# Kernel optimization log

Measured on AMD Instinct MI355X. Metric: run time of the kernel, lower is better.

The kernel has to match this reference:

```python
import jax, jax.numpy as jnp
import numpy as np

L, B, S, H, NH, HD = 2, 2, 1024, 768, 12, 64
E, K, F, V = 8, 2, 3072, 50257
THETA = 10000.0
EPS = 1e-5


def setup_inputs() -> dict:
    key = jax.random.key(0)
    ks = iter(jax.random.split(key, 40))
    def nrm(shape):
        return jax.random.normal(next(ks), shape, jnp.float32) * 0.02
    return {
        "input_ids": jax.random.randint(next(ks), (B, S), 0, V),
        "emb": nrm((V, H)),
        "ln1_w": jnp.ones((L, H)), "ln1_b": jnp.zeros((L, H)),
        "ln2_w": jnp.ones((L, H)), "ln2_b": jnp.zeros((L, H)),
        "lnf_w": jnp.ones((H,)), "lnf_b": jnp.zeros((H,)),
        "Wq": nrm((L, H, H)), "bq": jnp.zeros((L, H)),
        "Wk": nrm((L, H, H)), "bk": jnp.zeros((L, H)),
        "Wv": nrm((L, H, H)), "bv": jnp.zeros((L, H)),
        "Wo": nrm((L, H, H)), "bo": jnp.zeros((L, H)),
        "Wr": nrm((L, H, E)), "br": jnp.zeros((L, E)),
        "W1": nrm((L, E, H, F)), "b1": jnp.zeros((L, E, F)),
        "W2": nrm((L, E, F, H)), "b2": jnp.zeros((L, E, H)),
    }


def _layer_norm(x, w, b):
    m = x.mean(-1, keepdims=True)
    v = ((x - m) ** 2).mean(-1, keepdims=True)
    return (x - m) * jax.lax.rsqrt(v + EPS) * w + b


def _rotate_half(x):
    x1, x2 = jnp.split(x, 2, axis=-1)
    return jnp.concatenate([-x2, x1], axis=-1)


def _forward(input_ids, emb, ln1_w, ln1_b, ln2_w, ln2_b, lnf_w, lnf_b,
             Wq, bq, Wk, bk, Wv, bv, Wo, bo, Wr, br, W1, b1, W2, b2):
    x = emb[input_ids]  # [B,S,H]

    # RoPE tables [1,1,S,HD]
    inv_freq = 1.0 / (THETA ** (jnp.arange(0, HD, 2, dtype=jnp.float32) / HD))
    freqs = jnp.arange(S, dtype=jnp.float32)[:, None] * inv_freq[None, :]
    ang = jnp.concatenate([freqs, freqs], axis=-1)
    cos = jnp.cos(ang)[None, None].astype(x.dtype)
    sin = jnp.sin(ang)[None, None].astype(x.dtype)

    causal = jnp.where(jnp.tril(jnp.ones((S, S), dtype=bool)), 0.0, -1e9)
    causal = causal[None, None].astype(x.dtype)

    scale = 1.0 / np.sqrt(HD)
    for l in range(L):
        # --- attention block ---
        h = _layer_norm(x, ln1_w[l], ln1_b[l])
        q = (h @ Wq[l] + bq[l]).reshape(B, S, NH, HD).transpose(0, 2, 1, 3)
        k = (h @ Wk[l] + bk[l]).reshape(B, S, NH, HD).transpose(0, 2, 1, 3)
        v = (h @ Wv[l] + bv[l]).reshape(B, S, NH, HD).transpose(0, 2, 1, 3)
        q = q * cos + _rotate_half(q) * sin
        k = k * cos + _rotate_half(k) * sin
        scores = jnp.einsum('bhqd,bhkd->bhqk', q, k) * scale + causal
        attn = jax.nn.softmax(scores, axis=-1)
        o = jnp.einsum('bhqk,bhkd->bhqd', attn, v)
        o = o.transpose(0, 2, 1, 3).reshape(B, S, H)
        x = x + (o @ Wo[l] + bo[l])

        # --- MoE feed-forward block ---
        h = _layer_norm(x, ln2_w[l], ln2_b[l]).reshape(-1, H)  # [N,H]
        router_probs = jax.nn.softmax(h @ Wr[l] + br[l], axis=-1)  # [N,E]
        tp, ti = jax.lax.top_k(router_probs, K)
        tp = tp / (tp.sum(-1, keepdims=True) + 1e-9)
        # combine weights per expert (equiv. to the per-slot scatter loop)
        w = (jax.nn.one_hot(ti, E, dtype=h.dtype) * tp[..., None]).sum(1)  # [N,E]
        a = jax.nn.gelu(jnp.einsum('nh,ehf->nef', h, W1[l]) + b1[l], approximate=False)
        oe = jnp.einsum('nef,efh->neh', a, W2[l]) + b2[l]
        ff = jnp.einsum('ne,neh->nh', w, oe)
        x = x + ff.reshape(B, S, H)

    x = _layer_norm(x, lnf_w, lnf_b)
    logits = jnp.einsum('bsh,vh->bsv', x, emb)  # tied lm_head
    return logits


def reference(input_ids, emb, ln1_w, ln1_b, ln2_w, ln2_b, lnf_w, lnf_b,
              Wq, bq, Wk, bk, Wv, bv, Wo, bo, Wr, br, W1, b1, W2, b2):
    return _forward(input_ids, emb, ln1_w, ln1_b, ln2_w, ln2_b, lnf_w, lnf_b,
                    Wq, bq, Wk, bk, Wv, bv, Wo, bo, Wr, br, W1, b1, W2, b2)
```

## Files before the change

### kernel.cpp

```cpp
#include <hip/hip_runtime.h>
#include <stdint.h>

constexpr int L = 2, Bb = 2, S = 1024, H = 768, NHd = 12, HD = 64;
constexpr int E = 8, F = 3072, V = 50257;
constexpr int NTOK = Bb * S;
constexpr int NSLOT = NTOK * 2;
constexpr float EPSLN = 1e-5f;

typedef __attribute__((ext_vector_type(4))) float f32x4;
typedef __attribute__((ext_vector_type(8))) short s16x8;

#define DEVI __device__ __forceinline__

DEVI float bf2f(short u) {
  union { float f; uint32_t i; } c; c.i = ((uint32_t)(uint16_t)u) << 16; return c.f;
}
DEVI short f2bf(float f) {
  union { float f; uint32_t i; } c; c.f = f;
  uint32_t x = c.i;
  uint32_t r = (x + 0x7fffu + ((x >> 16) & 1u)) >> 16;
  return (short)r;
}

DEVI void gload16(const void* g, void* l) {
  __builtin_amdgcn_global_load_lds(g, l, 16, 0, 0);
}

DEVI float gelu1(float g) { return 0.5f * g * (1.f + erff(g * 0.70710678118f)); }

__global__ void k_f32_to_bf16(const float* __restrict__ in, short* __restrict__ out, long n4) {
  long i = (long)blockIdx.x * blockDim.x + threadIdx.x;
  if (i >= n4) return;
  long base = i * 4;
  f32x4 v = *(const f32x4*)(in + base);
  short4 o;
  o.x = f2bf(v.x); o.y = f2bf(v.y); o.z = f2bf(v.z); o.w = f2bf(v.w);
  *(short4*)(out + base) = o;
}

__global__ void k_transpose_bf16(const float* __restrict__ in, short* __restrict__ out,
                                 int R, int C, long inBS, long outBS) {
  __shared__ float tile[32][33];
  const float* src = in + (size_t)blockIdx.z * inBS;
  short* dst = out + (size_t)blockIdx.z * outBS;
  int r0 = blockIdx.y * 32, c0 = blockIdx.x * 32;
  int tx = threadIdx.x, ty = threadIdx.y;
#pragma unroll
  for (int i = 0; i < 32; i += 8) {
    int r = r0 + ty + i, c = c0 + tx;
    if (r < R && c < C) tile[ty + i][tx] = src[(size_t)r * C + c];
  }
  __syncthreads();
#pragma unroll
  for (int i = 0; i < 32; i += 8) {
    int c = c0 + ty + i, r = r0 + tx;
    if (r < R && c < C) dst[(size_t)c * R + r] = f2bf(tile[tx][ty + i]);
  }
}

__global__ void k_transpose_split(const float* __restrict__ in, short* __restrict__ oh,
                                  short* __restrict__ ol, int R, int C, long inBS,
                                  long outBS) {
  __shared__ float tile[32][33];
  const float* src = in + (size_t)blockIdx.z * inBS;
  short* dh = oh + (size_t)blockIdx.z * outBS;
  short* dl = ol + (size_t)blockIdx.z * outBS;
  int r0 = blockIdx.y * 32, c0 = blockIdx.x * 32;
  int tx = threadIdx.x, ty = threadIdx.y;
#pragma unroll
  for (int i = 0; i < 32; i += 8) {
    int r = r0 + ty + i, c = c0 + tx;
    if (r < R && c < C) tile[ty + i][tx] = src[(size_t)r * C + c];
  }
  __syncthreads();
#pragma unroll
  for (int i = 0; i < 32; i += 8) {
    int c = c0 + ty + i, r = r0 + tx;
    if (r < R && c < C) {
      float v = tile[tx][ty + i];
      short hi = f2bf(v);
      short lo = f2bf(v - bf2f(hi));
      dh[(size_t)c * R + r] = hi;
      dl[(size_t)c * R + r] = lo;
    }
  }
}

__global__ void k_transpose_split3(const float* __restrict__ in, short* __restrict__ o0,
                                   short* __restrict__ o1, short* __restrict__ o2,
                                   int R, int C) {
  __shared__ float tile[32][33];
  int r0 = blockIdx.y * 32, c0 = blockIdx.x * 32;
  int tx = threadIdx.x, ty = threadIdx.y;
#pragma unroll
  for (int i = 0; i < 32; i += 8) {
    int r = r0 + ty + i, c = c0 + tx;
    if (r < R && c < C) tile[ty + i][tx] = in[(size_t)r * C + c];
  }
  __syncthreads();
#pragma unroll
  for (int i = 0; i < 32; i += 8) {
    int c = c0 + ty + i, r = r0 + tx;
    if (r < R && c < C) {
      float v = tile[tx][ty + i];
      short t0 = f2bf(v);
      float rr = v - bf2f(t0);
      short t1 = f2bf(rr);
      short t2 = f2bf(rr - bf2f(t1));
      o0[(size_t)c * R + r] = t0;
      o1[(size_t)c * R + r] = t1;
      o2[(size_t)c * R + r] = t2;
    }
  }
}

__global__ void k_wqkv_t3(const float* __restrict__ Wq, const float* __restrict__ Wk,
                          const float* __restrict__ Wv, short* __restrict__ o0,
                          short* __restrict__ o1, short* __restrict__ o2) {
  __shared__ float tile[32][33];
  const int zz = blockIdx.z;
  const float* in = (zz == 0) ? Wq : (zz == 1) ? Wk : Wv;
  const size_t doff = (size_t)zz * H * H;
  int r0 = blockIdx.y * 32, c0 = blockIdx.x * 32;
  int tx = threadIdx.x, ty = threadIdx.y;
#pragma unroll
  for (int i = 0; i < 32; i += 8) {
    int r = r0 + ty + i, c = c0 + tx;
    tile[ty + i][tx] = in[(size_t)r * H + c];
  }
  __syncthreads();
#pragma unroll
  for (int i = 0; i < 32; i += 8) {
    int c = c0 + ty + i, r = r0 + tx;
    float v = tile[tx][ty + i];
    short t0 = f2bf(v);
    float rr = v - bf2f(t0);
    short t1 = f2bf(rr);
    short t2 = f2bf(rr - bf2f(t1));
    o0[doff + (size_t)c * H + r] = t0;
    o1[doff + (size_t)c * H + r] = t1;
    o2[doff + (size_t)c * H + r] = t2;
  }
}

__global__ void k_bqkv(const float* __restrict__ bq, const float* __restrict__ bk,
                       const float* __restrict__ bv, float* __restrict__ bqkv) {
  int i = blockIdx.x * blockDim.x + threadIdx.x;
  if (i >= L * 3 * H) return;
  int l = i / (3 * H), j = i % (3 * H);
  float v = (j < H) ? bq[l * H + j] : (j < 2 * H) ? bk[l * H + j - H] : bv[l * H + j - 2 * H];
  bqkv[i] = v;
}

__global__ void k_ropetab(float* __restrict__ cosT, float* __restrict__ sinT) {
  int i = blockIdx.x * blockDim.x + threadIdx.x;
  if (i >= S * (HD / 2)) return;
  int s = i / 32, d = i % 32;
  float invf = powf(10000.f, -(2.f * d) / (float)HD);
  float ang = (float)s * invf;
  cosT[i] = cosf(ang);
  sinT[i] = sinf(ang);
}

__global__ void k_embed(const int* __restrict__ ids, const float* __restrict__ emb,
                        float* __restrict__ x) {
  int idx = blockIdx.x * blockDim.x + threadIdx.x;
  int row = idx / (H / 4), c4 = idx % (H / 4);
  if (row >= NTOK) return;
  int t = ids[row];
  ((f32x4*)(x + (size_t)row * H))[c4] = ((const f32x4*)(emb + (size_t)t * H))[c4];
}

template <int OUT>
__global__ void k_layernorm(const float* __restrict__ x, const float* __restrict__ w,
                            const float* __restrict__ b, float* __restrict__ of,
                            short* __restrict__ s0, short* __restrict__ s1,
                            short* __restrict__ s2) {
  int row = blockIdx.x * (blockDim.x >> 6) + (threadIdx.x >> 6);
  int lane = threadIdx.x & 63;
  if (row >= NTOK) return;
  const float* xr = x + (size_t)row * H;
  float v[12], s = 0.f, s2s = 0.f;
#pragma unroll
  for (int j = 0; j < 12; j++) { float t = xr[lane + j * 64]; v[j] = t; s += t; s2s += t * t; }
#pragma unroll
  for (int off = 32; off; off >>= 1) { s += __shfl_xor(s, off); s2s += __shfl_xor(s2s, off); }
  float m = s / (float)H;
  float var = s2s / (float)H - m * m;
  float rs = 1.f / sqrtf(var + EPSLN);
#pragma unroll
  for (int j = 0; j < 12; j++) {
    int c = lane + j * 64;
    float val = (v[j] - m) * rs * w[c] + b[c];
    size_t idx = (size_t)row * H + c;
    if (OUT == 1) {
      short t0 = f2bf(val);
      float rr = val - bf2f(t0);
      short t1 = f2bf(rr);
      short t2 = f2bf(rr - bf2f(t1));
      s0[idx] = t0; s1[idx] = t1; s2[idx] = t2;
    } else if (OUT == 2) {
      of[idx] = val;
      short hi = f2bf(val);
      s0[idx] = hi; s1[idx] = f2bf(val - bf2f(hi));
    } else if (OUT == 3) {
      of[idx] = val;
      s0[idx] = f2bf(val);
    } else {
      s0[idx] = f2bf(val);
    }
  }
}

__global__ void k_softmax2(short* __restrict__ p0, short* __restrict__ p1) {
  int row = blockIdx.x * 4 + (threadIdx.x >> 6);
  int lane = threadIdx.x & 63;
  s16x8* r0 = (s16x8*)(p0 + (size_t)row * S + lane * 16);
  s16x8* r1 = (s16x8*)(p1 + (size_t)row * S + lane * 16);
  s16x8 h0 = r0[0], h1 = r0[1];
  s16x8 l0 = r1[0], l1 = r1[1];
  float v[16];
#pragma unroll
  for (int j = 0; j < 8; j++) {
    v[j] = bf2f(h0[j]) + bf2f(l0[j]);
    v[8 + j] = bf2f(h1[j]) + bf2f(l1[j]);
  }
  float mx = -3e38f;
#pragma unroll
  for (int j = 0; j < 16; j++) mx = fmaxf(mx, v[j]);
#pragma unroll
  for (int off = 32; off; off >>= 1) mx = fmaxf(mx, __shfl_xor(mx, off));
  float sum = 0.f;
#pragma unroll
  for (int j = 0; j < 16; j++) { v[j] = expf(v[j] - mx); sum += v[j]; }
#pragma unroll
  for (int off = 32; off; off >>= 1) sum += __shfl_xor(sum, off);
  float inv = 1.f / sum;
#pragma unroll
  for (int j = 0; j < 16; j++) v[j] *= inv;
  s16x8 oh0, oh1, ol0, ol1;
#pragma unroll
  for (int j = 0; j < 8; j++) {
    short hi = f2bf(v[j]);
    oh0[j] = hi; ol0[j] = f2bf(v[j] - bf2f(hi));
    short hi2 = f2bf(v[8 + j]);
    oh1[j] = hi2; ol1[j] = f2bf(v[8 + j] - bf2f(hi2));
  }
  r0[0] = oh0; r0[1] = oh1;
  r1[0] = ol0; r1[1] = ol1;
}

__global__ void k_router(const float* __restrict__ h, const float* __restrict__ Wr,
                         const float* __restrict__ br, float* __restrict__ sel_w,
                         int* __restrict__ sel_e, int* __restrict__ counts) {
  int tok = blockIdx.x * (blockDim.x >> 6) + (threadIdx.x >> 6);
  int lane = threadIdx.x & 63;
  if (tok >= NTOK) return;
  const float* hr = h + (size_t)tok * H;
  float acc[8] = {0, 0, 0, 0, 0, 0, 0, 0};
  for (int i = lane; i < H; i += 64) {
    float hv = hr[i];
    const f32x4* w4 = (const f32x4*)(Wr + (size_t)i * E);
    f32x4 a = w4[0], b = w4[1];
    acc[0] += hv * a.x; acc[1] += hv * a.y; acc[2] += hv * a.z; acc[3] += hv * a.w;
    acc[4] += hv * b.x; acc[5] += hv * b.y; acc[6] += hv * b.z; acc[7] += hv * b.w;
  }
#pragma unroll
  for (int off = 32; off; off >>= 1)
#pragma unroll
    for (int e = 0; e < 8; e++) acc[e] += __shfl_xor(acc[e], off);
  if (lane == 0) {
    float lg[8], m = -3e38f;
#pragma unroll
    for (int e = 0; e < 8; e++) { lg[e] = acc[e] + br[e]; m = fmaxf(m, lg[e]); }
    float sum = 0.f;
#pragma unroll
    for (int e = 0; e < 8; e++) { lg[e] = expf(lg[e] - m); sum += lg[e]; }
    float inv = 1.f / sum;
#pragma unroll
    for (int e = 0; e < 8; e++) lg[e] *= inv;
    int i1 = 0;
#pragma unroll
    for (int e = 1; e < 8; e++) if (lg[e] > lg[i1]) i1 = e;
    int i2 = (i1 == 0) ? 1 : 0;
#pragma unroll
    for (int e = 0; e < 8; e++) if (e != i1 && lg[e] > lg[i2]) i2 = e;
    float p1 = lg[i1], p2 = lg[i2];
    float ws = p1 + p2 + 1e-9f;
    sel_e[tok * 2] = i1; sel_e[tok * 2 + 1] = i2;
    sel_w[tok * 2] = p1 / ws; sel_w[tok * 2 + 1] = p2 / ws;
    atomicAdd(counts + i1, 1);
    atomicAdd(counts + i2, 1);
  }
}

__global__ void k_offsets(const int* __restrict__ counts, int* __restrict__ offs) {
  if (threadIdx.x == 0) {
    int a = 0;
    for (int e = 0; e < E; e++) { offs[e] = a; a += counts[e]; }
    offs[E] = a;
  }
}

__global__ void k_scatter(const int* __restrict__ sel_e, const int* __restrict__ offs,
                          int* __restrict__ cursor, int* __restrict__ tok_list,
                          int* __restrict__ slot_of) {
  int tok = blockIdx.x * blockDim.x + threadIdx.x;
  if (tok >= NTOK) return;
  for (int k = 0; k < 2; k++) {
    int e = sel_e[tok * 2 + k];
    int pos = atomicAdd(cursor + e, 1);
    int g = offs[e] + pos;
    tok_list[g] = tok;
    slot_of[tok * 2 + k] = g;
  }
}

__global__ void k_combine(const float* __restrict__ oe, const float* __restrict__ sel_w,
                          const int* __restrict__ slot_of, const int* __restrict__ sel_e,
                          const float* __restrict__ b2, float* __restrict__ x) {
  int idx = blockIdx.x * blockDim.x + threadIdx.x;
  if (idx >= NTOK * (H / 4)) return;
  int tok = idx / (H / 4), c4 = idx % (H / 4);
  float w0 = sel_w[tok * 2], w1 = sel_w[tok * 2 + 1];
  int s0 = slot_of[tok * 2], s1 = slot_of[tok * 2 + 1];
  int e0 = sel_e[tok * 2], e1 = sel_e[tok * 2 + 1];
  f32x4 a = ((const f32x4*)(oe + (size_t)s0 * H))[c4];
  f32x4 b = ((const f32x4*)(oe + (size_t)s1 * H))[c4];
  f32x4 ba = ((const f32x4*)(b2 + (size_t)e0 * H))[c4];
  f32x4 bb = ((const f32x4*)(b2 + (size_t)e1 * H))[c4];
  f32x4* xp = (f32x4*)(x + (size_t)tok * H) + c4;
  *xp = *xp + w0 * (a + ba) + w1 * (b + bb);
}

template <int SP, int MODE, bool GATHER>
__global__ __launch_bounds__(256, 2) void k_bgemmS(
    const short* __restrict__ A0, const short* __restrict__ A1, const short* __restrict__ A2,
    long sAz, int lda,
    const short* __restrict__ B0, const short* __restrict__ B1, const short* __restrict__ B2,
    long sBz, int ldb,
    void* __restrict__ Cp, void* __restrict__ Cp2, void* __restrict__ Cp3,
    short* __restrict__ K0, short* __restrict__ K1, short* __restrict__ K2,
    short* __restrict__ V0, short* __restrict__ V1,
    const float* __restrict__ cT, const float* __restrict__ sT,
    int zdiv, long sChi, long sClo, int ldc,
    const float* __restrict__ res, const float* __restrict__ bias, long sBias,
    int M, int N, int K,
    const int* __restrict__ d_counts, const int* __restrict__ d_offs,
    const int* __restrict__ gidx, float alpha) {
  const int z = blockIdx.z;
  const int Meff = d_counts ? d_counts[z] : M;
  const int tm = blockIdx.y;
  if (tm * 128 >= Meff) return;
  const int tn = blockIdx.x;
  const int row_base = d_offs ? d_offs[z] : 0;

  __shared__ short Ab[SP][128 * 32];
  __shared__ short Bb2[SP][128 * 32];

  const int tid = threadIdx.x;
  const int lane = tid & 63;
  const int w = tid >> 6;

  const short* APz[3];
  const short* BPz[3];
  APz[0] = A0 + (size_t)z * sAz;
  APz[1] = A1 + (size_t)z * sAz;
  APz[2] = (SP > 2) ? (A2 + (size_t)z * sAz) : APz[0];
  BPz[0] = B0 + (size_t)z * sBz;
  BPz[1] = B1 + (size_t)z * sBz;
  BPz[2] = (SP > 2) ? (B2 + (size_t)z * sBz) : BPz[0];

  size_t aOff[2], bOff[2];
#pragma unroll
  for (int i = 0; i < 2; ++i) {
    const int srow = i * 64 + (tid >> 2);
    const int kb = (tid & 3) ^ (srow & 3);
    int lrow = tm * 128 + srow;
    if (lrow > Meff - 1) lrow = Meff - 1;
    int ar = row_base + lrow;
    if (GATHER) ar = gidx[ar];
    aOff[i] = (size_t)ar * lda + kb * 8;
    int bcol = tn * 128 + srow;
    if (bcol > N - 1) bcol = N - 1;
    bOff[i] = (size_t)bcol * ldb + kb * 8;
  }

  f32x4 acc[4][4];
#pragma unroll
  for (int a = 0; a < 4; ++a)
#pragma unroll
    for (int b = 0; b < 4; ++b) acc[a][b] = {0.f, 0.f, 0.f, 0.f};

  const int wr = (w >> 1) * 64;
  const int wc = (w & 1) * 64;
  const int r16 = lane & 15;
  const int kb4 = lane >> 4;
  const int swz = (kb4 ^ (r16 & 3)) * 8;
  int aoff[4], boff[4];
#pragma unroll
  for (int i = 0; i < 4; ++i) {
    aoff[i] = (wr + i * 16 + r16) * 32 + swz;
    boff[i] = (wc + i * 16 + r16) * 32 + swz;
  }

  for (int k0 = 0; k0 < K; k0 += 32) {
#pragma unroll
    for (int s = 0; s < SP; ++s) {
      gload16(APz[s] + aOff[0], (char*)(&Ab[s][0]) + w * 1024);
      gload16(APz[s] + aOff[1], (char*)(&Ab[s][0]) + 4096 + w * 1024);
      gload16(BPz[s] + bOff[0], (char*)(&Bb2[s][0]) + w * 1024);
      gload16(BPz[s] + bOff[1], (char*)(&Bb2[s][0]) + 4096 + w * 1024);
    }
    aOff[0] += 32; aOff[1] += 32; bOff[0] += 32; bOff[1] += 32;
    __syncthreads();
    s16x8 af[SP][4], bf[SP][4];
#pragma unroll
    for (int s = 0; s < SP; ++s)
#pragma unroll
      for (int i = 0; i < 4; ++i) {
        af[s][i] = *(const s16x8*)(&Ab[s][aoff[i]]);
        bf[s][i] = *(const s16x8*)(&Bb2[s][boff[i]]);
      }
#pragma unroll
    for (int mi = 0; mi < 4; ++mi)
#pragma unroll
      for (int ni = 0; ni < 4; ++ni) {
        f32x4 a = acc[mi][ni];
#pragma unroll
        for (int si = 0; si < SP; ++si)
#pragma unroll
          for (int sj = 0; sj < SP - si; ++sj)
            a = __builtin_amdgcn_mfma_f32_16x16x32_bf16(af[si][mi], bf[sj][ni], a, 0, 0, 0);
        acc[mi][ni] = a;
      }
    __syncthreads();
  }

  const float* bz = bias ? (bias + (size_t)z * sBias) : nullptr;
  const int q4 = lane >> 4;
  float bvv[4];
  int gco[4];
#pragma unroll
  for (int ni = 0; ni < 4; ++ni) {
    gco[ni] = tn * 128 + wc + ni * 16 + r16;
    bvv[ni] = (bz && gco[ni] < N) ? bz[gco[ni]] : 0.f;
  }

  if (MODE == 9) {
    const int sec_base = tn * 128 + wc;
    const int sec = sec_base / H;
    const int hh = (sec_base % H) / HD;
#pragma unroll
    for (int mi = 0; mi < 4; ++mi) {
#pragma unroll
      for (int j = 0; j < 4; ++j) {
        const int row = tm * 128 + wr + mi * 16 + q4 * 4 + j;
        const int ss = row & (S - 1);
        const long zz = (long)((row >> 10) * NHd + hh);
#pragma unroll
        for (int ni = 0; ni < 2; ++ni) {
          const int d = ni * 16 + r16;
          float a1 = acc[mi][ni][j] + bvv[ni];
          float a2 = acc[mi][ni + 2][j] + bvv[ni + 2];
          if (sec < 2) {
            float cc = cT[ss * 32 + d], sn = sT[ss * 32 + d];
            float r1 = a1 * cc - a2 * sn;
            float r2 = a2 * cc + a1 * sn;
            const long bi = (zz * S + ss) * HD + d;
            short* d0 = (sec == 0) ? (short*)Cp : K0;
            short* d1 = (sec == 0) ? (short*)Cp2 : K1;
            short* d2 = (sec == 0) ? (short*)Cp3 : K2;
            short t0 = f2bf(r1); float rr = r1 - bf2f(t0);
            short t1 = f2bf(rr); short t2 = f2bf(rr - bf2f(t1));
            d0[bi] = t0; d1[bi] = t1; d2[bi] = t2;
            t0 = f2bf(r2); rr = r2 - bf2f(t0);
            t1 = f2bf(rr); t2 = f2bf(rr - bf2f(t1));
            d0[bi + 32] = t0; d1[bi + 32] = t1; d2[bi + 32] = t2;
          } else {
            const long vb1 = zz * HD * S + (long)d * S + ss;
            short hv = f2bf(a1);
            V0[vb1] = hv; V1[vb1] = f2bf(a1 - bf2f(hv));
            const long vb2 = vb1 + 32L * S;
            hv = f2bf(a2);
            V0[vb2] = hv; V1[vb2] = f2bf(a2 - bf2f(hv));
          }
        }
      }
    }
    return;
  }

  const long out_off = (long)(z / zdiv) * sChi + (long)(z % zdiv) * sClo;
#pragma unroll
  for (int mi = 0; mi < 4; ++mi) {
#pragma unroll
    for (int j = 0; j < 4; ++j) {
      const int lrow = tm * 128 + wr + mi * 16 + q4 * 4 + j;
      if (lrow >= Meff) continue;
      const long rbase = out_off + (long)(row_base + lrow) * ldc;
#pragma unroll
      for (int ni = 0; ni < 4; ++ni) {
        if (gco[ni] >= N) continue;
        const float v = acc[mi][ni][j];
        const long idx = rbase + gco[ni];
        if (MODE == 0) {
          ((float*)Cp)[idx] = v + bvv[ni];
        } else if (MODE == 1) {
          ((float*)Cp)[idx] = res[idx] + v + bvv[ni];
        } else if (MODE == 6) {
          float g = gelu1(v + bvv[ni]);
          short hi = f2bf(g);
          ((short*)Cp)[idx] = hi;
          ((short*)Cp2)[idx] = f2bf(g - bf2f(hi));
        } else if (MODE == 7) {
          float g = v * alpha + ((gco[ni] > lrow) ? -1e9f : 0.f);
          short hi = f2bf(g);
          ((short*)Cp)[idx] = hi;
          ((short*)Cp2)[idx] = f2bf(g - bf2f(hi));
        } else if (MODE == 8) {
          float g = v + bvv[ni];
          short t0 = f2bf(g); float rr = g - bf2f(t0);
          short t1 = f2bf(rr); short t2 = f2bf(rr - bf2f(t1));
          ((short*)Cp)[idx] = t0;
          ((short*)Cp2)[idx] = t1;
          ((short*)Cp3)[idx] = t2;
        }
      }
    }
  }
}

template <int SP, int MODE, bool GATHER>
static void bgemmS(hipStream_t st, const short* A0, const short* A1, const short* A2, long sAz,
                   int lda, const short* B0, const short* B1, const short* B2, long sBz,
                   int ldb, void* C, void* C2, void* C3, int zdiv, long sChi, long sClo,
                   int ldc, const float* res, const float* bias, long sBias, int M, int N,
                   int K, int nz, const int* cnts, const int* offs_, const int* gat,
                   float alpha, short* K0 = nullptr, short* K1 = nullptr, short* K2 = nullptr,
                   short* V0 = nullptr, short* V1 = nullptr, const float* cT = nullptr,
                   const float* sT = nullptr) {
  dim3 g((N + 127) / 128, (M + 127) / 128, nz);
  k_bgemmS<SP, MODE, GATHER><<<g, 256, 0, st>>>(A0, A1, A2, sAz, lda, B0, B1, B2, sBz, ldb, C,
                                                C2, C3, K0, K1, K2, V0, V1, cT, sT, zdiv, sChi,
                                                sClo, ldc, res, bias, sBias, M, N, K, cnts,
                                                offs_, gat, alpha);
}

template <int MODE, bool GATHER, bool NSWZ>
__global__ __launch_bounds__(256, 2) void k_bgemm(
    const short* __restrict__ A, long sAz, int lda,
    const short* __restrict__ Bt, long sBz, int ldb,
    void* __restrict__ Cp, int zdiv, long sChi, long sClo, int ldc,
    const float* __restrict__ bias, long sBias,
    int M, int N, int K,
    const int* __restrict__ d_counts, const int* __restrict__ d_offs,
    const int* __restrict__ gidx) {
  const int z = blockIdx.z;
  const int Meff = d_counts ? d_counts[z] : M;
  int tm, tn;
  if (NSWZ) {
    const int bid = blockIdx.y * gridDim.x + blockIdx.x;
    const int nwg = gridDim.x * gridDim.y;
    const int q = nwg >> 3, r = nwg & 7;
    const int xcd = bid & 7, ix = bid >> 3;
    const int wg = (xcd < r) ? (xcd * (q + 1) + ix) : (r * (q + 1) + (xcd - r) * q + ix);
    tn = wg / gridDim.y;
    tm = wg % gridDim.y;
  } else {
    tm = blockIdx.y;
    tn = blockIdx.x;
  }
  if (tm * 128 >= Meff) return;
  const int row_base = d_offs ? d_offs[z] : 0;

  __shared__ short Abuf[128 * 64];
  __shared__ short Bbuf[128 * 64];

  const int tid = threadIdx.x;
  const int lane = tid & 63;
  const int w = tid >> 6;

  const short* Az = A + (size_t)z * sAz;
  const short* Bz = Bt + (size_t)z * sBz;

  const int swzS = ((lane >> 3) ^ (lane & 7)) * 8;
  const short* aSrc[4];
  const short* bSrc[4];
#pragma unroll
  for (int i = 0; i < 4; ++i) {
    const int rin = (w * 4 + i) * 8 + (lane >> 3);
    int lrow = tm * 128 + rin;
    if (lrow > Meff - 1) lrow = Meff - 1;
    int ar = row_base + lrow;
    if (GATHER) ar = gidx[ar];
    aSrc[i] = Az + (size_t)ar * lda + swzS;
    int bcol = tn * 128 + rin;
    if (bcol > N - 1) bcol = N - 1;
    bSrc[i] = Bz + (size_t)bcol * ldb + swzS;
  }

  f32x4 acc[4][4];
#pragma unroll
  for (int a = 0; a < 4; ++a)
#pragma unroll
    for (int b = 0; b < 4; ++b) acc[a][b] = {0.f, 0.f, 0.f, 0.f};

  const int wr = (w >> 1) * 64;
  const int wc = (w & 1) * 64;
  const int r16 = lane & 15;
  const int kb4 = lane >> 4;
  int aoff[4][2], boff[4][2];
#pragma unroll
  for (int i = 0; i < 4; ++i) {
#pragma unroll
    for (int kw = 0; kw < 2; ++kw) {
      const int sw = ((r16 & 7) ^ (kw * 4 + kb4)) * 8;
      aoff[i][kw] = (wr + i * 16 + r16) * 64 + sw;
      boff[i][kw] = (wc + i * 16 + r16) * 64 + sw;
    }
  }

  for (int k0 = 0; k0 < K; k0 += 64) {
#pragma unroll
    for (int i = 0; i < 4; ++i) gload16(aSrc[i], (char*)Abuf + (w * 4 + i) * 1024);
#pragma unroll
    for (int i = 0; i < 4; ++i) gload16(bSrc[i], (char*)Bbuf + (w * 4 + i) * 1024);
#pragma unroll
    for (int i = 0; i < 4; ++i) { aSrc[i] += 64; bSrc[i] += 64; }
    __syncthreads();
#pragma unroll
    for (int kw = 0; kw < 2; ++kw) {
      s16x8 af[4], bf[4];
#pragma unroll
      for (int i = 0; i < 4; ++i) {
        af[i] = *(const s16x8*)(Abuf + aoff[i][kw]);
        bf[i] = *(const s16x8*)(Bbuf + boff[i][kw]);
      }
#pragma unroll
      for (int mi = 0; mi < 4; ++mi)
#pragma unroll
        for (int ni = 0; ni < 4; ++ni)
          acc[mi][ni] =
              __builtin_amdgcn_mfma_f32_16x16x32_bf16(af[mi], bf[ni], acc[mi][ni], 0, 0, 0);
    }
    __syncthreads();
  }

  const long out_off = (long)(z / zdiv) * sChi + (long)(z % zdiv) * sClo;
  const float* bz = bias ? (bias + (size_t)z * sBias) : nullptr;
  const int q4 = lane >> 4;
  float bvv[4];
  int gco[4];
#pragma unroll
  for (int ni = 0; ni < 4; ++ni) {
    gco[ni] = tn * 128 + wc + ni * 16 + r16;
    bvv[ni] = (bz && gco[ni] < N) ? bz[gco[ni]] : 0.f;
  }
#pragma unroll
  for (int mi = 0; mi < 4; ++mi) {
#pragma unroll
    for (int j = 0; j < 4; ++j) {
      const int lrow = tm * 128 + wr + mi * 16 + q4 * 4 + j;
      if (lrow >= Meff) continue;
      const long rbase = out_off + (row_base + lrow) * (long)ldc;
#pragma unroll
      for (int ni = 0; ni < 4; ++ni) {
        if (gco[ni] >= N) continue;
        const float v = acc[mi][ni][j];
        if (MODE == 0) {
          ((float*)Cp)[rbase + gco[ni]] = v + bvv[ni];
        } else if (MODE == 4) {
          float g = v + bvv[ni];
          ((short*)Cp)[rbase + gco[ni]] = f2bf(gelu1(g));
        }
      }
    }
  }
}

template <int MODE, bool GATHER, bool NSWZ>
static void bgemm(hipStream_t st, const short* A, long sAz, int lda, const short* Bt, long sBz,
                  int ldb, void* C, int zdiv, long sChi, long sClo, int ldc, const float* bias,
                  long sBias, int M, int N, int K, int nz, const int* cnts, const int* offs_,
                  const int* gat) {
  dim3 g((N + 127) / 128, (M + 127) / 128, nz);
  k_bgemm<MODE, GATHER, NSWZ><<<g, 256, 0, st>>>(A, sAz, lda, Bt, sBz, ldb, C, zdiv, sChi,
                                                 sClo, ldc, bias, sBias, M, N, K, cnts, offs_,
                                                 gat);
}

extern "C" void kernel_launch(void* const* d_in, const int* in_sizes, int n_in, void* d_out,
                              int out_size, void* d_ws, size_t ws_size, hipStream_t stream) {
  (void)in_sizes; (void)n_in; (void)out_size; (void)ws_size;
  const int*   ids  = (const int*)d_in[0];
  const float* emb  = (const float*)d_in[1];
  const float* ln1w = (const float*)d_in[2];
  const float* ln1b = (const float*)d_in[3];
  const float* ln2w = (const float*)d_in[4];
  const float* ln2b = (const float*)d_in[5];
  const float* lnfw = (const float*)d_in[6];
  const float* lnfb = (const float*)d_in[7];
  const float* Wq = (const float*)d_in[8];
  const float* bq = (const float*)d_in[9];
  const float* Wk = (const float*)d_in[10];
  const float* bk = (const float*)d_in[11];
  const float* Wv = (const float*)d_in[12];
  const float* bv = (const float*)d_in[13];
  const float* Wo = (const float*)d_in[14];
  const float* bo = (const float*)d_in[15];
  const float* Wr = (const float*)d_in[16];
  const float* br = (const float*)d_in[17];
  const float* W1 = (const float*)d_in[18];
  const float* b1 = (const float*)d_in[19];
  const float* W2 = (const float*)d_in[20];
  const float* b2 = (const float*)d_in[21];
  float* out = (float*)d_out;

  char* p = (char*)d_ws;
  auto alloc = [&](size_t bytes) {
    char* r = p;
    p += (bytes + 255) & ~(size_t)255;
    return r;
  };
  short* embB = (short*)alloc((size_t)V * H * 2);
  char* big = alloc((size_t)Bb * NHd * S * S * 2 * 2);
  short* p0   = (short*)big;
  short* p1   = p0 + (size_t)Bb * NHd * S * S;
  short* R_hi = (short*)big;
  short* R_lo = R_hi + (size_t)E * F * H;
  short* Wb0 = (short*)alloc((size_t)3 * H * H * 2);
  short* Wb1 = (short*)alloc((size_t)3 * H * H * 2);
  short* Wb2 = (short*)alloc((size_t)3 * H * H * 2);
  short* Wo0 = (short*)alloc((size_t)H * H * 2);
  short* Wo1 = (short*)alloc((size_t)H * H * 2);
  short* Wo2 = (short*)alloc((size_t)H * H * 2);
  float* bqkv = (float*)alloc((size_t)L * 3 * H * 4);
  float* cosT = (float*)alloc((size_t)S * 32 * 4);
  float* sinT = (float*)alloc((size_t)S * 32 * 4);
  float* x    = (float*)alloc((size_t)NTOK * H * 4);
  float* hbuf = (float*)alloc((size_t)NTOK * H * 4);
  short* xb   = (short*)alloc((size_t)NTOK * H * 2);
  short* xb2  = (short*)alloc((size_t)NTOK * H * 2);
  short* h_hi = (short*)alloc((size_t)NTOK * H * 2);
  short* h_lo = (short*)alloc((size_t)NTOK * H * 2);
  short* h30  = (short*)alloc((size_t)NTOK * H * 2);
  short* h31  = (short*)alloc((size_t)NTOK * H * 2);
  short* h32  = (short*)alloc((size_t)NTOK * H * 2);
  short* q30  = (short*)alloc((size_t)NTOK * H * 2);
  short* q31  = (short*)alloc((size_t)NTOK * H * 2);
  short* q32  = (short*)alloc((size_t)NTOK * H * 2);
  short* k30  = (short*)alloc((size_t)NTOK * H * 2);
  short* k31  = (short*)alloc((size_t)NTOK * H * 2);
  short* k32  = (short*)alloc((size_t)NTOK * H * 2);
  short* v20  = (short*)alloc((size_t)NTOK * H * 2);
  short* v21  = (short*)alloc((size_t)NTOK * H * 2);
  short* o30  = (short*)alloc((size_t)NTOK * H * 2);
  short* o31  = (short*)alloc((size_t)NTOK * H * 2);
  short* o32  = (short*)alloc((size_t)NTOK * H * 2);
  char* uni = alloc((size_t)NSLOT * F * 4 + (size_t)NSLOT * H * 4);
  short* act_hi = (short*)uni;
  short* act_lo = (short*)(uni + (size_t)NSLOT * F * 2);
  short* act_b  = (short*)uni;
  float* oe     = (float*)(uni + (size_t)NSLOT * F * 4);
  int* counts  = (int*)alloc(2 * E * 4);
  int* cursor  = counts + E;
  int* offs    = (int*)alloc((E + 1) * 4);
  int* sel_e   = (int*)alloc((size_t)NTOK * 2 * 4);
  float* sel_w = (float*)alloc((size_t)NTOK * 2 * 4);
  int* slot_of = (int*)alloc((size_t)NTOK * 2 * 4);
  int* tok_lst = (int*)alloc((size_t)NSLOT * 4);

  long nEmb4 = (long)V * H / 4;
  k_f32_to_bf16<<<(nEmb4 + 255) / 256, 256, 0, stream>>>(emb, embB, nEmb4);
  k_bqkv<<<(L * 3 * H + 255) / 256, 256, 0, stream>>>(bq, bk, bv, bqkv);
  k_ropetab<<<(S * 32 + 255) / 256, 256, 0, stream>>>(cosT, sinT);
  k_embed<<<(NTOK * (H / 4) + 255) / 256, 256, 0, stream>>>(ids, emb, x);

  dim3 tb(32, 8);
  const dim3 tHH(H / 32, H / 32, 1);

  for (int l = 0; l < L; l++) {
    k_layernorm<1><<<NTOK / 4, 256, 0, stream>>>(x, ln1w + l * H, ln1b + l * H, nullptr, h30,
                                                 h31, h32);
    k_wqkv_t3<<<dim3(H / 32, H / 32, 3), tb, 0, stream>>>(
        Wq + (size_t)l * H * H, Wk + (size_t)l * H * H, Wv + (size_t)l * H * H, Wb0, Wb1, Wb2);
    bgemmS<3, 9, false>(stream, h30, h31, h32, 0, H, Wb0, Wb1, Wb2, 0, H, q30, q31, q32, 1, 0,
                        0, 0, nullptr, bqkv + l * 3 * H, 0, NTOK, 3 * H, H, 1, nullptr,
                        nullptr, nullptr, 1.f, k30, k31, k32, v20, v21, cosT, sinT);
    bgemmS<3, 7, false>(stream, q30, q31, q32, (long)S * HD, HD, k30, k31, k32, (long)S * HD,
                        HD, p0, p1, nullptr, 1, (long)S * S, 0, S, nullptr, nullptr, 0, S, S,
                        HD, Bb * NHd, nullptr, nullptr, nullptr, 0.125f);
    k_softmax2<<<(Bb * NHd * S) / 4, 256, 0, stream>>>(p0, p1);
    bgemmS<2, 8, false>(stream, p0, p1, nullptr, (long)S * S, S, v20, v21, nullptr,
                        (long)HD * S, S, o30, o31, o32, NHd, (long)S * H, HD, H, nullptr,
                        nullptr, 0, S, HD, S, Bb * NHd, nullptr, nullptr, nullptr, 1.f);
    k_transpose_split3<<<tHH, tb, 0, stream>>>(Wo + (size_t)l * H * H, Wo0, Wo1, Wo2, H, H);
    bgemmS<3, 1, false>(stream, o30, o31, o32, 0, H, Wo0, Wo1, Wo2, 0, H, x, nullptr, nullptr,
                        1, 0, 0, H, x, bo + l * H, 0, NTOK, H, H, 1, nullptr, nullptr, nullptr,
                        1.f);

    if (l == 0)
      k_layernorm<2><<<NTOK / 4, 256, 0, stream>>>(x, ln2w + l * H, ln2b + l * H, hbuf, h_hi,
                                                   h_lo, nullptr);
    else
      k_layernorm<3><<<NTOK / 4, 256, 0, stream>>>(x, ln2w + l * H, ln2b + l * H, hbuf, xb2,
                                                   nullptr, nullptr);
    hipMemsetAsync(counts, 0, 2 * E * sizeof(int), stream);
    k_router<<<NTOK / 4, 256, 0, stream>>>(hbuf, Wr + (size_t)l * H * E, br + l * E, sel_w,
                                           sel_e, counts);
    k_offsets<<<1, 64, 0, stream>>>(counts, offs);
    k_scatter<<<(NTOK + 255) / 256, 256, 0, stream>>>(sel_e, offs, cursor, tok_lst, slot_of);
    if (l == 0) {
      k_transpose_split<<<dim3(F / 32, H / 32, E), tb, 0, stream>>>(
          W1, R_hi, R_lo, H, F, (long)H * F, (long)F * H);
      bgemmS<2, 6, true>(stream, h_hi, h_lo, nullptr, 0, H, R_hi, R_lo, nullptr, (long)F * H,
                         H, act_hi, act_lo, nullptr, 1, 0, 0, F, nullptr, b1, F, NSLOT, F, H,
                         E, counts, offs, tok_lst, 1.f);
      k_transpose_split<<<dim3(H / 32, F / 32, E), tb, 0, stream>>>(
          W2, R_hi, R_lo, F, H, (long)F * H, (long)H * F);
      bgemmS<2, 0, false>(stream, act_hi, act_lo, nullptr, 0, F, R_hi, R_lo, nullptr,
                          (long)H * F, F, oe, nullptr, nullptr, 1, 0, 0, H, nullptr, nullptr,
                          0, NSLOT, H, F, E, counts, offs, nullptr, 1.f);
      k_combine<<<(NTOK * (H / 4) + 255) / 256, 256, 0, stream>>>(oe, sel_w, slot_of, sel_e,
                                                                  b2, x);
    } else {
      k_transpose_bf16<<<dim3(F / 32, H / 32, E), tb, 0, stream>>>(
          W1 + (size_t)1 * E * H * F, R_hi, H, F, (long)H * F, (long)F * H);
      k_transpose_bf16<<<dim3(H / 32, F / 32, E), tb, 0, stream>>>(
          W2 + (size_t)1 * E * F * H, R_lo, F, H, (long)F * H, (long)H * F);
      bgemm<4, true, false>(stream, xb2, 0, H, R_hi, (long)F * H, H, act_b, 1, 0, 0, F,
                            b1 + (size_t)l * E * F, F, NSLOT, F, H, E, counts, offs, tok_lst);
      bgemm<0, false, false>(stream, act_b, 0, F, R_lo, (long)H * F, F, oe, 1, 0, 0, H,
                             nullptr, 0, NSLOT, H, F, E, counts, offs, nullptr);
      k_combine<<<(NTOK * (H / 4) + 255) / 256, 256, 0, stream>>>(oe, sel_w, slot_of, sel_e,
                                                                  b2 + (size_t)l * E * H, x);
    }
  }

  k_layernorm<4><<<NTOK / 4, 256, 0, stream>>>(x, lnfw, lnfb, nullptr, xb, nullptr, nullptr);
  bgemm<0, false, true>(stream, xb, 0, H, embB, 0, H, out, 1, 0, 0, V, nullptr, 0, NTOK, V, H,
                        1, nullptr, nullptr, nullptr);
}
```

Baseline: 1.700 ms.

## Drop third bf16 split term and skip masked causal blocks in attention

After: 1.578 ms (median of 2 runs). -7.2%, faster.

```diff
diff --git a/kernel.cpp b/kernel.cpp
--- a/kernel.cpp
+++ b/kernel.cpp
@@ -86,37 +86,9 @@
   }
 }
 
-__global__ void k_transpose_split3(const float* __restrict__ in, short* __restrict__ o0,
-                                   short* __restrict__ o1, short* __restrict__ o2,
-                                   int R, int C) {
-  __shared__ float tile[32][33];
-  int r0 = blockIdx.y * 32, c0 = blockIdx.x * 32;
-  int tx = threadIdx.x, ty = threadIdx.y;
-#pragma unroll
-  for (int i = 0; i < 32; i += 8) {
-    int r = r0 + ty + i, c = c0 + tx;
-    if (r < R && c < C) tile[ty + i][tx] = in[(size_t)r * C + c];
-  }
-  __syncthreads();
-#pragma unroll
-  for (int i = 0; i < 32; i += 8) {
-    int c = c0 + ty + i, r = r0 + tx;
-    if (r < R && c < C) {
-      float v = tile[tx][ty + i];
-      short t0 = f2bf(v);
-      float rr = v - bf2f(t0);
-      short t1 = f2bf(rr);
-      short t2 = f2bf(rr - bf2f(t1));
-      o0[(size_t)c * R + r] = t0;
-      o1[(size_t)c * R + r] = t1;
-      o2[(size_t)c * R + r] = t2;
-    }
-  }
-}
-
-__global__ void k_wqkv_t3(const float* __restrict__ Wq, const float* __restrict__ Wk,
+__global__ void k_wqkv_t2(const float* __restrict__ Wq, const float* __restrict__ Wk,
                           const float* __restrict__ Wv, short* __restrict__ o0,
-                          short* __restrict__ o1, short* __restrict__ o2) {
+                          short* __restrict__ o1) {
   __shared__ float tile[32][33];
   const int zz = blockIdx.z;
   const float* in = (zz == 0) ? Wq : (zz == 1) ? Wk : Wv;
@@ -134,12 +106,9 @@
     int c = c0 + ty + i, r = r0 + tx;
     float v = tile[tx][ty + i];
     short t0 = f2bf(v);
-    float rr = v - bf2f(t0);
-    short t1 = f2bf(rr);
-    short t2 = f2bf(rr - bf2f(t1));
+    short t1 = f2bf(v - bf2f(t0));
     o0[doff + (size_t)c * H + r] = t0;
     o1[doff + (size_t)c * H + r] = t1;
-    o2[doff + (size_t)c * H + r] = t2;
   }
 }
 
@@ -174,8 +143,7 @@
 template <int OUT>
 __global__ void k_layernorm(const float* __restrict__ x, const float* __restrict__ w,
                             const float* __restrict__ b, float* __restrict__ of,
-                            short* __restrict__ s0, short* __restrict__ s1,
-                            short* __restrict__ s2) {
+                            short* __restrict__ s0, short* __restrict__ s1) {
   int row = blockIdx.x * (blockDim.x >> 6) + (threadIdx.x >> 6);
   int lane = threadIdx.x & 63;
   if (row >= NTOK) return;
@@ -195,10 +163,7 @@
     size_t idx = (size_t)row * H + c;
     if (OUT == 1) {
       short t0 = f2bf(val);
-      float rr = val - bf2f(t0);
-      short t1 = f2bf(rr);
-      short t2 = f2bf(rr - bf2f(t1));
-      s0[idx] = t0; s1[idx] = t1; s2[idx] = t2;
+      s0[idx] = t0; s1[idx] = f2bf(val - bf2f(t0));
     } else if (OUT == 2) {
       of[idx] = val;
       short hi = f2bf(val);
@@ -215,39 +180,49 @@
 __global__ void k_softmax2(short* __restrict__ p0, short* __restrict__ p1) {
   int row = blockIdx.x * 4 + (threadIdx.x >> 6);
   int lane = threadIdx.x & 63;
-  s16x8* r0 = (s16x8*)(p0 + (size_t)row * S + lane * 16);
-  s16x8* r1 = (s16x8*)(p1 + (size_t)row * S + lane * 16);
-  s16x8 h0 = r0[0], h1 = r0[1];
-  s16x8 l0 = r1[0], l1 = r1[1];
+  const int nb = ((row & (S - 1)) >> 7) + 1;
+  const size_t base = (size_t)row * S;
   float v[16];
-#pragma unroll
-  for (int j = 0; j < 8; j++) {
-    v[j] = bf2f(h0[j]) + bf2f(l0[j]);
-    v[8 + j] = bf2f(h1[j]) + bf2f(l1[j]);
-  }
   float mx = -3e38f;
 #pragma unroll
-  for (int j = 0; j < 16; j++) mx = fmaxf(mx, v[j]);
+  for (int c = 0; c < 8; ++c) {
+    if (c < nb) {
+      uint32_t u0 = *(const uint32_t*)(p0 + base + c * 128 + lane * 2);
+      uint32_t u1 = *(const uint32_t*)(p1 + base + c * 128 + lane * 2);
+      float a = bf2f((short)(u0 & 0xffff)) + bf2f((short)(u1 & 0xffff));
+      float b = bf2f((short)(u0 >> 16)) + bf2f((short)(u1 >> 16));
+      v[c * 2] = a; v[c * 2 + 1] = b;
+      mx = fmaxf(mx, fmaxf(a, b));
+    }
+  }
 #pragma unroll
   for (int off = 32; off; off >>= 1) mx = fmaxf(mx, __shfl_xor(mx, off));
   float sum = 0.f;
 #pragma unroll
-  for (int j = 0; j < 16; j++) { v[j] = expf(v[j] - mx); sum += v[j]; }
+  for (int c = 0; c < 8; ++c) {
+    if (c < nb) {
+      float a = expf(v[c * 2] - mx);
+      float b = expf(v[c * 2 + 1] - mx);
+      v[c * 2] = a; v[c * 2 + 1] = b;
+      sum += a + b;
+    }
+  }
 #pragma unroll
   for (int off = 32; off; off >>= 1) sum += __shfl_xor(sum, off);
   float inv = 1.f / sum;
 #pragma unroll
-  for (int j = 0; j < 16; j++) v[j] *= inv;
-  s16x8 oh0, oh1, ol0, ol1;
-#pragma unroll
-  for (int j = 0; j < 8; j++) {
-    short hi = f2bf(v[j]);
-    oh0[j] = hi; ol0[j] = f2bf(v[j] - bf2f(hi));
-    short hi2 = f2bf(v[8 + j]);
-    oh1[j] = hi2; ol1[j] = f2bf(v[8 + j] - bf2f(hi2));
-  }
-  r0[0] = oh0; r0[1] = oh1;
-  r1[0] = ol0; r1[1] = ol1;
+  for (int c = 0; c < 8; ++c) {
+    if (c < nb) {
+      float a = v[c * 2] * inv;
+      float b = v[c * 2 + 1] * inv;
+      short ah = f2bf(a), bh = f2bf(b);
+      short al = f2bf(a - bf2f(ah)), bl = f2bf(b - bf2f(bh));
+      *(uint32_t*)(p0 + base + c * 128 + lane * 2) =
+          (uint32_t)(uint16_t)ah | ((uint32_t)(uint16_t)bh << 16);
+      *(uint32_t*)(p1 + base + c * 128 + lane * 2) =
+          (uint32_t)(uint16_t)al | ((uint32_t)(uint16_t)bl << 16);
+    }
+  }
 }
 
 __global__ void k_router(const float* __restrict__ h, const float* __restrict__ Wr,
@@ -339,8 +314,8 @@
     long sAz, int lda,
     const short* __restrict__ B0, const short* __restrict__ B1, const short* __restrict__ B2,
     long sBz, int ldb,
-    void* __restrict__ Cp, void* __restrict__ Cp2, void* __restrict__ Cp3,
-    short* __restrict__ K0, short* __restrict__ K1, short* __restrict__ K2,
+    void* __restrict__ Cp, void* __restrict__ Cp2,
+    short* __restrict__ K0, short* __restrict__ K1,
     short* __restrict__ V0, short* __restrict__ V1,
     const float* __restrict__ cT, const float* __restrict__ sT,
     int zdiv, long sChi, long sClo, int ldc,
@@ -355,12 +330,20 @@
   const int tn = blockIdx.x;
   const int row_base = d_offs ? d_offs[z] : 0;
 
+  if (MODE == 7 && tn > tm) return;
+
   __shared__ short Ab[SP][128 * 32];
   __shared__ short Bb2[SP][128 * 32];
 
   const int tid = threadIdx.x;
   const int lane = tid & 63;
   const int w = tid >> 6;
+
+  const int wr = (w >> 1) * 64;
+  const int wc = (w & 1) * 64;
+  const int r16 = lane & 15;
+  const int kb4 = lane >> 4;
+  const int q4 = lane >> 4;
 
   const short* APz[3];
   const short* BPz[3];
@@ -392,10 +375,6 @@
 #pragma unroll
     for (int b = 0; b < 4; ++b) acc[a][b] = {0.f, 0.f, 0.f, 0.f};
 
-  const int wr = (w >> 1) * 64;
-  const int wc = (w & 1) * 64;
-  const int r16 = lane & 15;
-  const int kb4 = lane >> 4;
   const int swz = (kb4 ^ (r16 & 3)) * 8;
   int aoff[4], boff[4];
 #pragma unroll
@@ -404,7 +383,9 @@
     boff[i] = (wc + i * 16 + r16) * 32 + swz;
   }
 
-  for (int k0 = 0; k0 < K; k0 += 32) {
+  const int Keff = (MODE == 8) ? (((tm + 1) * 128 < K) ? (tm + 1) * 128 : K) : K;
+
+  for (int k0 = 0; k0 < Keff; k0 += 32) {
 #pragma unroll
     for (int s = 0; s < SP; ++s) {
       gload16(APz[s] + aOff[0], (char*)(&Ab[s][0]) + w * 1024);
@@ -438,7 +419,6 @@
   }
 
   const float* bz = bias ? (bias + (size_t)z * sBias) : nullptr;
-  const int q4 = lane >> 4;
   float bvv[4];
   int gco[4];
 #pragma unroll
@@ -470,13 +450,10 @@
             const long bi = (zz * S + ss) * HD + d;
             short* d0 = (sec == 0) ? (short*)Cp : K0;
             short* d1 = (sec == 0) ? (short*)Cp2 : K1;
-            short* d2 = (sec == 0) ? (short*)Cp3 : K2;
-            short t0 = f2bf(r1); float rr = r1 - bf2f(t0);
-            short t1 = f2bf(rr); short t2 = f2bf(rr - bf2f(t1));
-            d0[bi] = t0; d1[bi] = t1; d2[bi] = t2;
-            t0 = f2bf(r2); rr = r2 - bf2f(t0);
-            t1 = f2bf(rr); t2 = f2bf(rr - bf2f(t1));
-            d0[bi + 32] = t0; d1[bi + 32] = t1; d2[bi + 32] = t2;
+            short t0 = f2bf(r1);
+            d0[bi] = t0; d1[bi] = f2bf(r1 - bf2f(t0));
+            t0 = f2bf(r2);
+            d0[bi + 32] = t0; d1[bi + 32] = f2bf(r2 - bf2f(t0));
           } else {
             const long vb1 = zz * HD * S + (long)d * S + ss;
             short hv = f2bf(a1);
@@ -520,11 +497,9 @@
           ((short*)Cp2)[idx] = f2bf(g - bf2f(hi));
         } else if (MODE == 8) {
           float g = v + bvv[ni];
-          short t0 = f2bf(g); float rr = g - bf2f(t0);
-          short t1 = f2bf(rr); short t2 = f2bf(rr - bf2f(t1));
+          short t0 = f2bf(g);
           ((short*)Cp)[idx] = t0;
-          ((short*)Cp2)[idx] = t1;
-          ((short*)Cp3)[idx] = t2;
+          ((short*)Cp2)[idx] = f2bf(g - bf2f(t0));
         }
       }
     }
@@ -534,15 +509,15 @@
 template <int SP, int MODE, bool GATHER>
 static void bgemmS(hipStream_t st, const short* A0, const short* A1, const short* A2, long sAz,
                    int lda, const short* B0, const short* B1, const short* B2, long sBz,
-                   int ldb, void* C, void* C2, void* C3, int zdiv, long sChi, long sClo,
+                   int ldb, void* C, void* C2, int zdiv, long sChi, long sClo,
                    int ldc, const float* res, const float* bias, long sBias, int M, int N,
                    int K, int nz, const int* cnts, const int* offs_, const int* gat,
-                   float alpha, short* K0 = nullptr, short* K1 = nullptr, short* K2 = nullptr,
+                   float alpha, short* K0 = nullptr, short* K1 = nullptr,
                    short* V0 = nullptr, short* V1 = nullptr, const float* cT = nullptr,
                    const float* sT = nullptr) {
   dim3 g((N + 127) / 128, (M + 127) / 128, nz);
   k_bgemmS<SP, MODE, GATHER><<<g, 256, 0, st>>>(A0, A1, A2, sAz, lda, B0, B1, B2, sBz, ldb, C,
-                                                C2, C3, K0, K1, K2, V0, V1, cT, sT, zdiv, sChi,
+                                                C2, K0, K1, V0, V1, cT, sT, zdiv, sChi,
                                                 sClo, ldc, res, bias, sBias, M, N, K, cnts,
                                                 offs_, gat, alpha);
 }
@@ -731,10 +706,8 @@
   short* R_lo = R_hi + (size_t)E * F * H;
   short* Wb0 = (short*)alloc((size_t)3 * H * H * 2);
   short* Wb1 = (short*)alloc((size_t)3 * H * H * 2);
-  short* Wb2 = (short*)alloc((size_t)3 * H * H * 2);
   short* Wo0 = (short*)alloc((size_t)H * H * 2);
   short* Wo1 = (short*)alloc((size_t)H * H * 2);
-  short* Wo2 = (short*)alloc((size_t)H * H * 2);
   float* bqkv = (float*)alloc((size_t)L * 3 * H * 4);
   float* cosT = (float*)alloc((size_t)S * 32 * 4);
   float* sinT = (float*)alloc((size_t)S * 32 * 4);
@@ -746,18 +719,14 @@
   short* h_lo = (short*)alloc((size_t)NTOK * H * 2);
   short* h30  = (short*)alloc((size_t)NTOK * H * 2);
   short* h31  = (short*)alloc((size_t)NTOK * H * 2);
-  short* h32  = (short*)alloc((size_t)NTOK * H * 2);
   short* q30  = (short*)alloc((size_t)NTOK * H * 2);
   short* q31  = (short*)alloc((size_t)NTOK * H * 2);
-  short* q32  = (short*)alloc((size_t)NTOK * H * 2);
   short* k30  = (short*)alloc((size_t)NTOK * H * 2);
   short* k31  = (short*)alloc((size_t)NTOK * H * 2);
-  short* k32  = (short*)alloc((size_t)NTOK * H * 2);
   short* v20  = (short*)alloc((size_t)NTOK * H * 2);
   short* v21  = (short*)alloc((size_t)NTOK * H * 2);
   short* o30  = (short*)alloc((size_t)NTOK * H * 2);
   short* o31  = (short*)alloc((size_t)NTOK * H * 2);
-  short* o32  = (short*)alloc((size_t)NTOK * H * 2);
   char* uni = alloc((size_t)NSLOT * F * 4 + (size_t)NSLOT * H * 4);
   short* act_hi = (short*)uni;
   short* act_lo = (short*)(uni + (size_t)NSLOT * F * 2);
@@ -782,30 +751,30 @@
 
   for (int l = 0; l < L; l++) {
     k_layernorm<1><<<NTOK / 4, 256, 0, stream>>>(x, ln1w + l * H, ln1b + l * H, nullptr, h30,
-                                                 h31, h32);
-    k_wqkv_t3<<<dim3(H / 32, H / 32, 3), tb, 0, stream>>>(
-        Wq + (size_t)l * H * H, Wk + (size_t)l * H * H, Wv + (size_t)l * H * H, Wb0, Wb1, Wb2);
-    bgemmS<3, 9, false>(stream, h30, h31, h32, 0, H, Wb0, Wb1, Wb2, 0, H, q30, q31, q32, 1, 0,
-                        0, 0, nullptr, bqkv + l * 3 * H, 0, NTOK, 3 * H, H, 1, nullptr,
-                        nullptr, nullptr, 1.f, k30, k31, k32, v20, v21, cosT, sinT);
-    bgemmS<3, 7, false>(stream, q30, q31, q32, (long)S * HD, HD, k30, k31, k32, (long)S * HD,
-                        HD, p0, p1, nullptr, 1, (long)S * S, 0, S, nullptr, nullptr, 0, S, S,
-                        HD, Bb * NHd, nullptr, nullptr, nullptr, 0.125f);
+                                                 h31);
+    k_wqkv_t2<<<dim3(H / 32, H / 32, 3), tb, 0, stream>>>(
+        Wq + (size_t)l * H * H, Wk + (size_t)l * H * H, Wv + (size_t)l * H * H, Wb0, Wb1);
+    bgemmS<2, 9, false>(stream, h30, h31, nullptr, 0, H, Wb0, Wb1, nullptr, 0, H, q30, q31,
+                        1, 0, 0, 0, nullptr, bqkv + l * 3 * H, 0, NTOK, 3 * H, H, 1, nullptr,
+                        nullptr, nullptr, 1.f, k30, k31, v20, v21, cosT, sinT);
+    bgemmS<2, 7, false>(stream, q30, q31, nullptr, (long)S * HD, HD, k30, k31, nullptr,
+                        (long)S * HD, HD, p0, p1, 1, (long)S * S, 0, S, nullptr, nullptr, 0,
+                        S, S, HD, Bb * NHd, nullptr, nullptr, nullptr, 0.125f);
     k_softmax2<<<(Bb * NHd * S) / 4, 256, 0, stream>>>(p0, p1);
     bgemmS<2, 8, false>(stream, p0, p1, nullptr, (long)S * S, S, v20, v21, nullptr,
-                        (long)HD * S, S, o30, o31, o32, NHd, (long)S * H, HD, H, nullptr,
+                        (long)HD * S, S, o30, o31, NHd, (long)S * H, HD, H, nullptr,
                         nullptr, 0, S, HD, S, Bb * NHd, nullptr, nullptr, nullptr, 1.f);
-    k_transpose_split3<<<tHH, tb, 0, stream>>>(Wo + (size_t)l * H * H, Wo0, Wo1, Wo2, H, H);
-    bgemmS<3, 1, false>(stream, o30, o31, o32, 0, H, Wo0, Wo1, Wo2, 0, H, x, nullptr, nullptr,
+    k_transpose_split<<<tHH, tb, 0, stream>>>(Wo + (size_t)l * H * H, Wo0, Wo1, H, H, 0, 0);
+    bgemmS<2, 1, false>(stream, o30, o31, nullptr, 0, H, Wo0, Wo1, nullptr, 0, H, x, nullptr,
                         1, 0, 0, H, x, bo + l * H, 0, NTOK, H, H, 1, nullptr, nullptr, nullptr,
                         1.f);
 
     if (l == 0)
       k_layernorm<2><<<NTOK / 4, 256, 0, stream>>>(x, ln2w + l * H, ln2b + l * H, hbuf, h_hi,
-                                                   h_lo, nullptr);
+                                                   h_lo);
     else
       k_layernorm<3><<<NTOK / 4, 256, 0, stream>>>(x, ln2w + l * H, ln2b + l * H, hbuf, xb2,
-                                                   nullptr, nullptr);
+                                                   nullptr);
     hipMemsetAsync(counts, 0, 2 * E * sizeof(int), stream);
     k_router<<<NTOK / 4, 256, 0, stream>>>(hbuf, Wr + (size_t)l * H * E, br + l * E, sel_w,
                                            sel_e, counts);
@@ -815,12 +784,12 @@
       k_transpose_split<<<dim3(F / 32, H / 32, E), tb, 0, stream>>>(
           W1, R_hi, R_lo, H, F, (long)H * F, (long)F * H);
       bgemmS<2, 6, true>(stream, h_hi, h_lo, nullptr, 0, H, R_hi, R_lo, nullptr, (long)F * H,
-                         H, act_hi, act_lo, nullptr, 1, 0, 0, F, nullptr, b1, F, NSLOT, F, H,
+                         H, act_hi, act_lo, 1, 0, 0, F, nullptr, b1, F, NSLOT, F, H,
                          E, counts, offs, tok_lst, 1.f);
       k_transpose_split<<<dim3(H / 32, F / 32, E), tb, 0, stream>>>(
           W2, R_hi, R_lo, F, H, (long)F * H, (long)H * F);
       bgemmS<2, 0, false>(stream, act_hi, act_lo, nullptr, 0, F, R_hi, R_lo, nullptr,
-                          (long)H * F, F, oe, nullptr, nullptr, 1, 0, 0, H, nullptr, nullptr,
+                          (long)H * F, F, oe, nullptr, 1, 0, 0, H, nullptr, nullptr,
                           0, NSLOT, H, F, E, counts, offs, nullptr, 1.f);
       k_combine<<<(NTOK * (H / 4) + 255) / 256, 256, 0, stream>>>(oe, sel_w, slot_of, sel_e,
                                                                   b2, x);
@@ -838,7 +807,7 @@
     }
   }
 
-  k_layernorm<4><<<NTOK / 4, 256, 0, stream>>>(x, lnfw, lnfb, nullptr, xb, nullptr, nullptr);
+  k_layernorm<4><<<NTOK / 4, 256, 0, stream>>>(x, lnfw, lnfb, nullptr, xb, nullptr);
   bgemm<0, false, true>(stream, xb, 0, H, embB, 0, H, out, 1, 0, 0, V, nullptr, 0, NTOK, V, H,
                         1, nullptr, nullptr, nullptr);
 }
```
